# Kernel optimization log

Hardware: AMD Instinct MI355X
Metric: run time of the kernel (lower is better)

Reference implementation:

```python
import jax, jax.numpy as jnp
import numpy as np

# ---- constants from SystemsOfSprings.f ----
TS = 0.05                      # integration step h
K_G, C_G = 1.0, 2.0            # ground spring / damper (k1..k4, c1..c4)
K_I, C_I = 1.0, 0.0            # inter-agent spring / damper (k5..k10, c5..c10)
_L9 = float(np.sqrt(4.0 ** 2 + 1.5 ** 2))
EDGE_I = jnp.array([0, 1, 2, 3, 2, 3])          # springs 5,6,7,8,9,10
EDGE_J = jnp.array([1, 2, 3, 0, 0, 1])
EDGE_L = jnp.array([4.0, 1.5, 4.0, 1.5, _L9, _L9], dtype=jnp.float32)
XBAR = jnp.array([2.0, 2.0, 0.0, 0.0, -2.0, 2.0, 0.0, 0.0,
                  -2.0, -2.0, 0.0, 0.0, 2.0, -2.0, 0.0, 0.0], dtype=jnp.float32)


def _step(x, u, xbar):
    # x: (16,) = [px,py,vx,vy] x 4 agents; u: (8,) = 2 force inputs per agent
    px, py, vx, vy = x[0::4], x[1::4], x[2::4], x[3::4]      # (4,) each (Mx/My/Mvx/Mvy selections)
    xt, yt = xbar[0::4], xbar[1::4]

    # ground spring + damper forces (toward target, opposing velocity)
    dxt, dyt = px - xt, py - yt
    ang_t = jnp.arctan2(dyt, dxt)
    ang_v = jnp.arctan2(vy, vx)
    Fk0 = K_G * jnp.sqrt(dxt ** 2 + dyt ** 2)
    Fc0 = C_G * jnp.sqrt(vx ** 2 + vy ** 2)
    Fgx = -Fk0 * jnp.cos(ang_t) - Fc0 * jnp.cos(ang_v)
    Fgy = -Fk0 * jnp.sin(ang_t) - Fc0 * jnp.sin(ang_v)

    # inter-agent springs/dampers on the 6 edges (edge list, no 4x4 diagonal NaNs)
    dxe = px[EDGE_I] - px[EDGE_J]
    dye = py[EDGE_I] - py[EDGE_J]
    dvxe = vx[EDGE_I] - vx[EDGE_J]
    dvye = vy[EDGE_I] - vy[EDGE_J]
    Fke = K_I * (jnp.sqrt(dxe ** 2 + dye ** 2) - EDGE_L)
    Fce = C_I * jnp.sqrt(dvxe ** 2 + dvye ** 2)
    ang = jnp.arctan2(dye, dxe)      # angle from j toward i's perspective at i
    angv = jnp.arctan2(dvye, dvxe)
    cxe, sye = jnp.cos(ang), jnp.sin(ang)
    cve, sve = jnp.cos(angv), jnp.sin(angv)
    # force on agent i: -F*proj(i,j); on agent j: -F*proj(j,i) = +F*proj(i,j)
    z4 = jnp.zeros(4, x.dtype)
    Fsx = z4.at[EDGE_I].add(-Fke * cxe).at[EDGE_J].add(Fke * cxe)
    Fsy = z4.at[EDGE_I].add(-Fke * sye).at[EDGE_J].add(Fke * sye)
    Fdx = z4.at[EDGE_I].add(-Fce * cve).at[EDGE_J].add(Fce * cve)
    Fdy = z4.at[EDGE_I].add(-Fce * sve).at[EDGE_J].add(Fce * sve)

    accx = Fsx + Fdx + Fgx  # masses m1..m4 = 1
    accy = Fsy + Fdy + Fgy

    dx = jnp.zeros(16, x.dtype)
    dx = dx.at[0::4].set(vx).at[1::4].set(vy).at[2::4].set(accx).at[3::4].set(accy)
    Bu = jnp.zeros(16, x.dtype).at[2::4].set(u[0::2]).at[3::4].set(u[1::2])
    return x + (dx + Bu) * TS


def setup_inputs() -> dict:
    key = jax.random.key(0)
    kx, ku = jax.random.split(key)
    B = 1048576
    x = jax.random.normal(kx, (B, 16), dtype=jnp.float32)
    u = jax.random.normal(ku, (B, 8), dtype=jnp.float32)
    return {"t": 0, "x": x, "u": u, "w": jnp.zeros((16,), jnp.float32), "xbar": XBAR}


def reference(t, x, u, w, xbar):
    # t and w are unused, exactly as in the torch forward; batch via vmap
    return jax.vmap(lambda xi, ui: _step(xi, ui, xbar))(x, u)
```

## Files before the change

kernel.cpp:

```cpp
#include <hip/hip_runtime.h>


#define TS 0.05f
#define NELEM 4

template<int CTRL>
__device__ __forceinline__ float qp(float v) {
    return __int_as_float(__builtin_amdgcn_update_dpp(
        0, __float_as_int(v), CTRL, 0xF, 0xF, true));
}

__device__ __forceinline__ void edge(float px, float py, float qx, float qy,
                                     float L, float& ax, float& ay) {
    float dx = px - qx;
    float dy = py - qy;
    float d2 = fmaf(dx, dx, dy * dy);
    float invr = __builtin_amdgcn_rsqf(d2);
    float s = fmaf(-L, invr, 1.0f);
    bool nz = d2 > 0.f;
    float fx = nz ? dx * s : -L;
    float fy = nz ? dy * s : 0.f;
    ax -= fx;
    ay -= fy;
}

__global__ __launch_bounds__(256) void springs_node_kernel(
    const float* __restrict__ x,
    const float* __restrict__ u,
    float* __restrict__ out,
    int N)
{
    const int t = threadIdx.x;
    const int base = blockIdx.x * (256 * NELEM) + t;
    const int node = t & 3;

    const float xt = (node == 1 || node == 2) ? -2.f : 2.f;
    const float yt = (node >= 2) ? -2.f : 2.f;

    const float4* x4 = reinterpret_cast<const float4*>(x);
    const float2* u2 = reinterpret_cast<const float2*>(u);
    float4*       o4 = reinterpret_cast<float4*>(out);

    float4 s[NELEM];
    float2 uc[NELEM];
    bool   ok[NELEM];

#pragma unroll
    for (int e = 0; e < NELEM; ++e) {
        int g = base + e * 256;
        ok[e] = (g < N);
        if (ok[e]) {
            s[e]  = x4[g];
            uc[e] = u2[g];
        }
    }

#pragma unroll
    for (int e = 0; e < NELEM; ++e) {
        float px = s[e].x, py = s[e].y, vx = s[e].z, vy = s[e].w;

        float ax = -(px - xt) - 2.f * vx;
        float ay = -(py - yt) - 2.f * vy;

        edge(px, py, qp<0xB1>(px), qp<0xB1>(py), 4.0f,          ax, ay);
        edge(px, py, qp<0x4E>(px), qp<0x4E>(py), 4.2720018727f, ax, ay);
        edge(px, py, qp<0x1B>(px), qp<0x1B>(py), 1.5f,          ax, ay);

        float4 r;
        r.x = fmaf(TS, vx, px);
        r.y = fmaf(TS, vy, py);
        r.z = fmaf(TS, ax + uc[e].x, vx);
        r.w = fmaf(TS, ay + uc[e].y, vy);

        if (ok[e]) {
            int g = base + e * 256;
            o4[g] = r;
        }
    }
}

extern "C" void kernel_launch(void* const* d_in, const int* in_sizes, int n_in,
                              void* d_out, int out_size, void* d_ws, size_t ws_size,
                              hipStream_t stream) {
    const float* x = (const float*)d_in[1];
    const float* u = (const float*)d_in[2];
    float* out = (float*)d_out;

    int N = in_sizes[1] / 4;
    int per_block = 256 * NELEM;
    int grid = (N + per_block - 1) / per_block;
    springs_node_kernel<<<grid, 256, 0, stream>>>(x, u, out, N);
}
```

Measured before the change: 147.9 us.

## Map two agents per thread with 16-byte loads and nontemporal stores

Each thread now owns two agents of a system instead of one, so the two-agent state is read as two float4 loads and the u pair as one float4 load. This cuts cross-lane DPP traffic to a single quad swizzle and halves the number of threads. Output is written with nontemporal stores to avoid polluting cache. In exchange, each memory access instruction now has a 32-byte per-thread stride pattern for x, and there are fewer threads in flight per block.

```diff
diff --git a/kernel.cpp b/kernel.cpp
--- a/kernel.cpp
+++ b/kernel.cpp
@@ -2,7 +2,10 @@
 
 
 #define TS 0.05f
-#define NELEM 4
+#define L9 4.2720018727f
+#define NELEM 2
+
+typedef float vf4 __attribute__((ext_vector_type(4)));
 
 template<int CTRL>
 __device__ __forceinline__ float qp(float v) {
@@ -10,84 +13,99 @@
         0, __float_as_int(v), CTRL, 0xF, 0xF, true));
 }
 
-__device__ __forceinline__ void edge(float px, float py, float qx, float qy,
-                                     float L, float& ax, float& ay) {
+__device__ __forceinline__ void edge1(float px, float py, float qx, float qy,
+                                      float L, float& ax, float& ay) {
     float dx = px - qx;
     float dy = py - qy;
     float d2 = fmaf(dx, dx, dy * dy);
     float invr = __builtin_amdgcn_rsqf(d2);
     float s = fmaf(-L, invr, 1.0f);
     bool nz = d2 > 0.f;
-    float fx = nz ? dx * s : -L;
-    float fy = nz ? dy * s : 0.f;
-    ax -= fx;
-    ay -= fy;
+    ax -= nz ? dx * s : -L;
+    ay -= nz ? dy * s : 0.f;
 }
 
-__global__ __launch_bounds__(256) void springs_node_kernel(
-    const float* __restrict__ x,
-    const float* __restrict__ u,
-    float* __restrict__ out,
-    int N)
+__device__ __forceinline__ void compute_pair(
+    const vf4& s0, const vf4& s1, const vf4& uu,
+    float xt0, float yt0, float xt1, float yt1,
+    vf4& r0, vf4& r1)
+{
+    float p0x = s0.x, p0y = s0.y, v0x = s0.z, v0y = s0.w;
+    float p1x = s1.x, p1y = s1.y, v1x = s1.z, v1y = s1.w;
+
+    float q0x = qp<0xB1>(p0x), q0y = qp<0xB1>(p0y);
+    float q1x = qp<0xB1>(p1x), q1y = qp<0xB1>(p1y);
+
+    float a0x = -(p0x - xt0) - 2.f * v0x;
+    float a0y = -(p0y - yt0) - 2.f * v0y;
+    float a1x = -(p1x - xt1) - 2.f * v1x;
+    float a1y = -(p1y - yt1) - 2.f * v1y;
+
+    edge1(p0x, p0y, p1x, p1y, 4.0f, a0x, a0y);
+    edge1(p0x, p0y, q0x, q0y, L9,   a0x, a0y);
+    edge1(p0x, p0y, q1x, q1y, 1.5f, a0x, a0y);
+    edge1(p1x, p1y, p0x, p0y, 4.0f, a1x, a1y);
+    edge1(p1x, p1y, q0x, q0y, 1.5f, a1x, a1y);
+    edge1(p1x, p1y, q1x, q1y, L9,   a1x, a1y);
+
+    r0.x = fmaf(TS, v0x, p0x);
+    r0.y = fmaf(TS, v0y, p0y);
+    r0.z = fmaf(TS, a0x + uu.x, v0x);
+    r0.w = fmaf(TS, a0y + uu.y, v0y);
+    r1.x = fmaf(TS, v1x, p1x);
+    r1.y = fmaf(TS, v1y, p1y);
+    r1.z = fmaf(TS, a1x + uu.z, v1x);
+    r1.w = fmaf(TS, a1y + uu.w, v1y);
+}
+
+__global__ __launch_bounds__(256) void springs_pair_kernel(
+    const vf4* __restrict__ x4,
+    const vf4* __restrict__ u4,
+    vf4* __restrict__ o4,
+    int NP)
 {
     const int t = threadIdx.x;
     const int base = blockIdx.x * (256 * NELEM) + t;
-    const int node = t & 3;
 
-    const float xt = (node == 1 || node == 2) ? -2.f : 2.f;
-    const float yt = (node >= 2) ? -2.f : 2.f;
+    const int par = t & 1;
+    const float xt0 = par ? -2.f : 2.f;
+    const float yt0 = par ? -2.f : 2.f;
+    const float xt1 = -xt0;
+    const float yt1 = yt0;
 
-    const float4* x4 = reinterpret_cast<const float4*>(x);
-    const float2* u2 = reinterpret_cast<const float2*>(u);
-    float4*       o4 = reinterpret_cast<float4*>(out);
+    const int g0 = min(base,       NP - 1);
+    const int g1 = min(base + 256, NP - 1);
 
-    float4 s[NELEM];
-    float2 uc[NELEM];
-    bool   ok[NELEM];
+    vf4 s00 = x4[2 * g0];
+    vf4 s01 = x4[2 * g0 + 1];
+    vf4 ua  = u4[g0];
+    vf4 s10 = x4[2 * g1];
+    vf4 s11 = x4[2 * g1 + 1];
+    vf4 ub  = u4[g1];
 
-#pragma unroll
-    for (int e = 0; e < NELEM; ++e) {
-        int g = base + e * 256;
-        ok[e] = (g < N);
-        if (ok[e]) {
-            s[e]  = x4[g];
-            uc[e] = u2[g];
-        }
+    vf4 r00, r01, r10, r11;
+    compute_pair(s00, s01, ua, xt0, yt0, xt1, yt1, r00, r01);
+    compute_pair(s10, s11, ub, xt0, yt0, xt1, yt1, r10, r11);
+
+    if (base < NP) {
+        __builtin_nontemporal_store(r00, &o4[2 * base]);
+        __builtin_nontemporal_store(r01, &o4[2 * base + 1]);
     }
-
-#pragma unroll
-    for (int e = 0; e < NELEM; ++e) {
-        float px = s[e].x, py = s[e].y, vx = s[e].z, vy = s[e].w;
-
-        float ax = -(px - xt) - 2.f * vx;
-        float ay = -(py - yt) - 2.f * vy;
-
-        edge(px, py, qp<0xB1>(px), qp<0xB1>(py), 4.0f,          ax, ay);
-        edge(px, py, qp<0x4E>(px), qp<0x4E>(py), 4.2720018727f, ax, ay);
-        edge(px, py, qp<0x1B>(px), qp<0x1B>(py), 1.5f,          ax, ay);
-
-        float4 r;
-        r.x = fmaf(TS, vx, px);
-        r.y = fmaf(TS, vy, py);
-        r.z = fmaf(TS, ax + uc[e].x, vx);
-        r.w = fmaf(TS, ay + uc[e].y, vy);
-
-        if (ok[e]) {
-            int g = base + e * 256;
-            o4[g] = r;
-        }
+    if (base + 256 < NP) {
+        __builtin_nontemporal_store(r10, &o4[2 * (base + 256)]);
+        __builtin_nontemporal_store(r11, &o4[2 * (base + 256) + 1]);
     }
 }
 
 extern "C" void kernel_launch(void* const* d_in, const int* in_sizes, int n_in,
                               void* d_out, int out_size, void* d_ws, size_t ws_size,
                               hipStream_t stream) {
-    const float* x = (const float*)d_in[1];
-    const float* u = (const float*)d_in[2];
-    float* out = (float*)d_out;
+    const vf4* x4 = (const vf4*)d_in[1];
+    const vf4* u4 = (const vf4*)d_in[2];
+    vf4* o4 = (vf4*)d_out;
 
-    int N = in_sizes[1] / 4;
+    int NP = in_sizes[1] / 8;
     int per_block = 256 * NELEM;
-    int grid = (N + per_block - 1) / per_block;
-    springs_node_kernel<<<grid, 256, 0, stream>>>(x, u, out, N);
+    int grid = (NP + per_block - 1) / per_block;
+    springs_pair_kernel<<<grid, 256, 0, stream>>>(x4, u4, o4, NP);
 }
```

Measured after the change: 151.8 us. +2.7%, slower.

## Switch to grid-stride persistent kernel with software-pipelined prefetch loads

Applied to the files above, without the earlier changes.

Replaces the one-shot kernel (4 elements per thread, one block per 1024 node rows) with a fixed grid of 2048 blocks that walk the data with a grid stride. Each iteration loads the next row before computing and storing the current one, so load latency overlaps with compute. This cuts block launch overhead and keeps a steady memory stream, at the cost of less memory-level parallelism per thread than issuing 4 independent loads at once. The DPP quad-neighbour logic stays valid because the stride is a multiple of 4.

```diff
diff --git a/kernel.cpp b/kernel.cpp
--- a/kernel.cpp
+++ b/kernel.cpp
@@ -2,7 +2,10 @@
 
 
 #define TS 0.05f
-#define NELEM 4
+#define L9 4.2720018727f
+
+typedef float vf4 __attribute__((ext_vector_type(4)));
+typedef float vf2 __attribute__((ext_vector_type(2)));
 
 template<int CTRL>
 __device__ __forceinline__ float qp(float v) {
@@ -10,84 +13,81 @@
         0, __float_as_int(v), CTRL, 0xF, 0xF, true));
 }
 
-__device__ __forceinline__ void edge(float px, float py, float qx, float qy,
-                                     float L, float& ax, float& ay) {
+__device__ __forceinline__ void edge1(float px, float py, float qx, float qy,
+                                      float L, float& ax, float& ay) {
     float dx = px - qx;
     float dy = py - qy;
     float d2 = fmaf(dx, dx, dy * dy);
     float invr = __builtin_amdgcn_rsqf(d2);
     float s = fmaf(-L, invr, 1.0f);
     bool nz = d2 > 0.f;
-    float fx = nz ? dx * s : -L;
-    float fy = nz ? dy * s : 0.f;
-    ax -= fx;
-    ay -= fy;
+    ax -= nz ? dx * s : -L;
+    ay -= nz ? dy * s : 0.f;
 }
 
-__global__ __launch_bounds__(256) void springs_node_kernel(
-    const float* __restrict__ x,
-    const float* __restrict__ u,
-    float* __restrict__ out,
+__device__ __forceinline__ vf4 step(vf4 s, vf2 uc, float xt, float yt) {
+    float px = s.x, py = s.y, vx = s.z, vy = s.w;
+
+    float ax = -(px - xt) - 2.f * vx;
+    float ay = -(py - yt) - 2.f * vy;
+
+    edge1(px, py, qp<0xB1>(px), qp<0xB1>(py), 4.0f, ax, ay);
+    edge1(px, py, qp<0x4E>(px), qp<0x4E>(py), L9,   ax, ay);
+    edge1(px, py, qp<0x1B>(px), qp<0x1B>(py), 1.5f, ax, ay);
+
+    vf4 r;
+    r.x = fmaf(TS, vx, px);
+    r.y = fmaf(TS, vy, py);
+    r.z = fmaf(TS, ax + uc.x, vx);
+    r.w = fmaf(TS, ay + uc.y, vy);
+    return r;
+}
+
+__global__ __launch_bounds__(256) void springs_stream_kernel(
+    const vf4* __restrict__ x4,
+    const vf2* __restrict__ u2,
+    vf4* __restrict__ o4,
     int N)
 {
     const int t = threadIdx.x;
-    const int base = blockIdx.x * (256 * NELEM) + t;
     const int node = t & 3;
-
     const float xt = (node == 1 || node == 2) ? -2.f : 2.f;
     const float yt = (node >= 2) ? -2.f : 2.f;
 
-    const float4* x4 = reinterpret_cast<const float4*>(x);
-    const float2* u2 = reinterpret_cast<const float2*>(u);
-    float4*       o4 = reinterpret_cast<float4*>(out);
+    const int S = gridDim.x * 256;
+    int g = blockIdx.x * 256 + t;
+    const int full = N / S;
 
-    float4 s[NELEM];
-    float2 uc[NELEM];
-    bool   ok[NELEM];
-
-#pragma unroll
-    for (int e = 0; e < NELEM; ++e) {
-        int g = base + e * 256;
-        ok[e] = (g < N);
-        if (ok[e]) {
-            s[e]  = x4[g];
-            uc[e] = u2[g];
+    if (full > 0) {
+        vf4 s0 = x4[g];
+        vf2 u0 = u2[g];
+        int gc = g;
+        for (int k = 1; k < full; ++k) {
+            int gn = gc + S;
+            vf4 s1 = x4[gn];
+            vf2 u1 = u2[gn];
+            o4[gc] = step(s0, u0, xt, yt);
+            s0 = s1; u0 = u1; gc = gn;
         }
+        o4[gc] = step(s0, u0, xt, yt);
     }
 
-#pragma unroll
-    for (int e = 0; e < NELEM; ++e) {
-        float px = s[e].x, py = s[e].y, vx = s[e].z, vy = s[e].w;
-
-        float ax = -(px - xt) - 2.f * vx;
-        float ay = -(py - yt) - 2.f * vy;
-
-        edge(px, py, qp<0xB1>(px), qp<0xB1>(py), 4.0f,          ax, ay);
-        edge(px, py, qp<0x4E>(px), qp<0x4E>(py), 4.2720018727f, ax, ay);
-        edge(px, py, qp<0x1B>(px), qp<0x1B>(py), 1.5f,          ax, ay);
-
-        float4 r;
-        r.x = fmaf(TS, vx, px);
-        r.y = fmaf(TS, vy, py);
-        r.z = fmaf(TS, ax + uc[e].x, vx);
-        r.w = fmaf(TS, ay + uc[e].y, vy);
-
-        if (ok[e]) {
-            int g = base + e * 256;
-            o4[g] = r;
-        }
+    int gt = g + full * S;
+    if (gt < N) {
+        o4[gt] = step(x4[gt], u2[gt], xt, yt);
     }
 }
 
 extern "C" void kernel_launch(void* const* d_in, const int* in_sizes, int n_in,
                               void* d_out, int out_size, void* d_ws, size_t ws_size,
                               hipStream_t stream) {
-    const float* x = (const float*)d_in[1];
-    const float* u = (const float*)d_in[2];
-    float* out = (float*)d_out;
+    const vf4* x4 = (const vf4*)d_in[1];
+    const vf2* u2 = (const vf2*)d_in[2];
+    vf4* o4 = (vf4*)d_out;
 
     int N = in_sizes[1] / 4;
-    int per_block = 256 * NELEM;
-    int grid = (N + per_block - 1) / per_block;
-    springs_node_kernel<<<grid, 256, 0, stream>>>(x, u, out, N);
+    int grid = 2048;
+    int max_needed = (N + 255) / 256;
+    if (grid > max_needed) grid = max_needed;
+    springs_stream_kernel<<<grid, 256, 0, stream>>>(x4, u2, o4, N);
 }
```

New measurement: 148.5 us. No clear change (+0.4%).
